# Kernel optimization log

Hardware: AMD Instinct MI355X
Metric: run time of the kernel (lower is better)

Reference implementation:

```python
import jax, jax.numpy as jnp
import numpy as np

B, S, D, H, L = 128, 200, 512, 512, 2  # batch, seq(=max_seq_len), input, hidden, layers


def _uni(key, shape, fan):
    bound = 1.0 / np.sqrt(fan)
    return jax.random.uniform(key, shape, jnp.float32, -bound, bound)


def setup_inputs() -> dict:
    key = jax.random.key(0)
    ks = jax.random.split(key, 12)
    x = jax.random.normal(ks[0], (B, S, D), jnp.float32)
    lens = jax.random.randint(ks[1], (B,), 1, S + 1).astype(jnp.int64)
    return {
        'x': x,
        'lens': lens,
        'Wih_f': _uni(ks[2], (L, 4 * H, D), H),
        'Whh_f': _uni(ks[3], (L, 4 * H, H), H),
        'bih_f': _uni(ks[4], (L, 4 * H), H),
        'bhh_f': _uni(ks[5], (L, 4 * H), H),
        'Wih_b': _uni(ks[6], (L, 4 * H, D), H),
        'Whh_b': _uni(ks[7], (L, 4 * H, H), H),
        'bih_b': _uni(ks[8], (L, 4 * H), H),
        'bhh_b': _uni(ks[9], (L, 4 * H), H),
    }


def _lstm_dir(xs, Wih, Whh, bih, bhh, reverse):
    # xs: [B,S,Din]. Precompute batched input projection, scan the recurrence.
    gx = jnp.einsum('bsd,gd->bsg', xs, Wih) + bih  # [B,S,4H]
    h0 = jnp.zeros((xs.shape[0], Whh.shape[1]), xs.dtype)
    c0 = jnp.zeros_like(h0)

    def step(carry, g_t):
        h, c = carry
        gates = g_t + h @ Whh.T + bhh
        i, f, g, o = jnp.split(gates, 4, axis=-1)  # PyTorch LSTMCell order
        i = jax.nn.sigmoid(i)
        f = jax.nn.sigmoid(f)
        g = jnp.tanh(g)
        o = jax.nn.sigmoid(o)
        c = f * c + i * g
        h = o * jnp.tanh(c)
        return (h, c), h

    _, hs = jax.lax.scan(step, (h0, c0), jnp.swapaxes(gx, 0, 1), reverse=reverse)
    return jnp.swapaxes(hs, 0, 1)  # [B,S,H], time-ordered


def reference(x, lens, Wih_f, Whh_f, bih_f, bhh_f, Wih_b, Whh_b, bih_b, bhh_b):
    valid = (jnp.arange(S)[None, :] < lens[:, None]).astype(x.dtype)[..., None]  # [B,S,1]
    f_in, b_in = x, x
    for l in range(L):
        f_h = _lstm_dir(f_in, Wih_f[l], Whh_f[l], bih_f[l], bhh_f[l], reverse=False)
        b_h = _lstm_dir(b_in, Wih_b[l], Whh_b[l], bih_b[l], bhh_b[l], reverse=True)
        f_h = f_h * valid  # masked_fill(mask, 0) for positions >= lens
        b_h = b_h * valid
        f_in, b_in = f_h, b_h
    return jnp.concatenate((f_in, b_in), axis=2)  # [B,S,2H]
```

## Files before the change

### kernel.cpp

```cpp
#include <hip/hip_runtime.h>
#include <hip/hip_bf16.h>

typedef __bf16 bf16x8 __attribute__((ext_vector_type(8)));
typedef _Float16 f16x8 __attribute__((ext_vector_type(8)));
typedef float f32x4 __attribute__((ext_vector_type(4)));

__device__ __forceinline__ unsigned short f2bf(float f) {
    unsigned int u = __builtin_bit_cast(unsigned int, f);
    u += 0x7FFFu + ((u >> 16) & 1u);
    return (unsigned short)(u >> 16);
}
__device__ __forceinline__ float bf2f(unsigned short s) {
    unsigned int u = ((unsigned int)s) << 16;
    return __builtin_bit_cast(float, u);
}

__device__ __forceinline__ void ldg_c(uint4& d, const void* p) {
    asm volatile("global_load_dwordx4 %0, %1, off sc0 sc1" : "=v"(d) : "v"(p));
}
__device__ __forceinline__ void stg_c32(void* p, unsigned v) {
    asm volatile("global_store_dword %0, %1, off sc0 sc1" :: "v"(p), "v"(v) : "memory");
}
__device__ __forceinline__ void vm_drain() {
    asm volatile("s_waitcnt vmcnt(0)" ::: "memory");
    __builtin_amdgcn_sched_barrier(0);
}
__device__ __forceinline__ void lds_fence() {
    asm volatile("s_waitcnt lgkmcnt(0)" ::: "memory");
    __builtin_amdgcn_sched_barrier(0);
}

__device__ __forceinline__ void wait_flags(const unsigned* f, unsigned tgt) {
    int lane = threadIdx.x & 63;
    for (;;) {
        unsigned v = __hip_atomic_load(f + lane, __ATOMIC_RELAXED, __HIP_MEMORY_SCOPE_AGENT);
        if (__all((int)(v >= tgt))) break;
        __builtin_amdgcn_s_sleep(1);
    }
}

__global__ void prep_x(const float* __restrict__ x,
                       unsigned short* __restrict__ xh,
                       unsigned short* __restrict__ xl) {
    int g = blockIdx.x * 256 + threadIdx.x;
    if (g >= 1638400) return;
    int lane = g & 63;
    int kc   = (g >> 6) & 15;
    int nt   = (g >> 10) & 7;
    int t    = g >> 13;
    int batch = nt * 16 + (lane & 15);
    int k = kc * 32 + (lane >> 4) * 8;
    const float* s = x + ((size_t)batch * 200 + t) * 512 + k;
    float4 v0 = *(const float4*)s;
    float4 v1 = *(const float4*)(s + 4);
    float vv[8] = {v0.x, v0.y, v0.z, v0.w, v1.x, v1.y, v1.z, v1.w};
    unsigned int ph[4], pl[4];
    #pragma unroll
    for (int j = 0; j < 4; ++j) {
        float a = vv[2*j], b = vv[2*j+1];
        unsigned short ha = f2bf(a), hb = f2bf(b);
        unsigned short la = f2bf(a - bf2f(ha)), lb = f2bf(b - bf2f(hb));
        ph[j] = (unsigned)ha | ((unsigned)hb << 16);
        pl[j] = (unsigned)la | ((unsigned)lb << 16);
    }
    ((uint4*)xh)[g] = make_uint4(ph[0], ph[1], ph[2], ph[3]);
    ((uint4*)xl)[g] = make_uint4(pl[0], pl[1], pl[2], pl[3]);
}

__global__ void prep_w(const float* __restrict__ W,
                       unsigned short* __restrict__ wprep,
                       int dir, int isHH) {
    int g = blockIdx.x * 256 + threadIdx.x;
    if (g >= 262144) return;
    int lane = g & 63;
    int kc   = (g >> 6) & 15;
    int mt   = (g >> 10) & 1;
    int cu   = (g >> 11) & 63;
    int l    = g >> 17;
    int r = lane & 15;
    int grow = (2 * mt + (r >> 3)) * 512 + cu * 8 + (r & 7);
    int k = kc * 32 + (lane >> 4) * 8;
    const float* s = W + ((size_t)l * 2048 + grow) * 512 + k;
    float4 v0 = *(const float4*)s;
    float4 v1 = *(const float4*)(s + 4);
    float vv[8] = {v0.x, v0.y, v0.z, v0.w, v1.x, v1.y, v1.z, v1.w};
    bool f16fmt = isHH || (l == 1);
    unsigned int ph[4], pl[4];
    #pragma unroll
    for (int j = 0; j < 4; ++j) {
        float a = vv[2*j], b = vv[2*j+1];
        unsigned short ha, hb, la, lb;
        if (f16fmt) {
            _Float16 fa = (_Float16)a, fb = (_Float16)b;
            _Float16 ra = (_Float16)(a - (float)fa), rb = (_Float16)(b - (float)fb);
            ha = __builtin_bit_cast(unsigned short, fa);
            hb = __builtin_bit_cast(unsigned short, fb);
            la = __builtin_bit_cast(unsigned short, ra);
            lb = __builtin_bit_cast(unsigned short, rb);
        } else {
            ha = f2bf(a); hb = f2bf(b);
            la = f2bf(a - bf2f(ha)); lb = f2bf(b - bf2f(hb));
        }
        ph[j] = (unsigned)ha | ((unsigned)hb << 16);
        pl[j] = (unsigned)la | ((unsigned)lb << 16);
    }
    size_t blk = ((size_t)(dir * 2 + l) * 64 + cu) * 8192;
    size_t fH = blk + (size_t)((isHH * 2 + 0) * 2048 + mt * 1024 + kc * 64 + lane);
    size_t fL = blk + (size_t)((isHH * 2 + 1) * 2048 + mt * 1024 + kc * 64 + lane);
    ((uint4*)wprep)[fH] = make_uint4(ph[0], ph[1], ph[2], ph[3]);
    ((uint4*)wprep)[fL] = make_uint4(pl[0], pl[1], pl[2], pl[3]);
}

__global__ void bsum_k(const float* __restrict__ bih_f, const float* __restrict__ bhh_f,
                       const float* __restrict__ bih_b, const float* __restrict__ bhh_b,
                       float* __restrict__ bsum) {
    int i = blockIdx.x * 256 + threadIdx.x;
    if (i < 8192) {
        int dir = i >> 12, rem = i & 4095;
        const float* bi = dir ? bih_b : bih_f;
        const float* bh = dir ? bhh_b : bhh_f;
        bsum[i] = bi[rem] + bh[rem];
    }
}

__global__ void reset_k(uint4* __restrict__ p) {
    int g = blockIdx.x * 256 + threadIdx.x;
    if (g < 131136) p[g] = make_uint4(0, 0, 0, 0);
}

__global__ void __launch_bounds__(512)
lstm_persist(const unsigned short* __restrict__ xh,
             const unsigned short* __restrict__ xl,
             const unsigned short* __restrict__ wprep,
             const float*          __restrict__ bsum,
             unsigned short*       __restrict__ hbuf,
             const int*            __restrict__ lens,
             float*                __restrict__ dout,
             unsigned*             __restrict__ flagv)
{
    extern __shared__ char smem[];
    float* wexch  = (float*)(smem + 131072);
    float* cst    = (float*)(smem + 131072 + 17408);
    float* bias_l = (float*)(smem + 131072 + 17408 + 4224);

    const int bid  = blockIdx.x;
    const int xcd  = bid & 7;
    const int unit = xcd >> 1;
    const int slot = unit >> 1, dir = unit & 1;
    const int cu8  = ((xcd & 1) << 5) | (bid >> 3);
    const int hj0  = cu8 * 8;
    const int tid  = threadIdx.x;
    const int lane = tid & 63, ng = tid >> 6;
    const int l15  = lane & 15, kg = lane >> 4;
    const int wsel = dir * 2 + slot;

    const int sib = slot ? dir : (2 + dir);
    unsigned* own_f = flagv + unit * 64;
    unsigned* sib_f = flagv + sib * 64;

    {
        const uint4* src = (const uint4*)wprep + ((size_t)(wsel * 64 + cu8) * 8192);
        uint4* dst = (uint4*)smem;
        #pragma unroll
        for (int i = 0; i < 16; ++i) dst[tid + i * 512] = src[tid + i * 512];
    }
    for (int i = tid; i < 8 * 132; i += 512) cst[i] = 0.f;
    if (tid < 32) bias_l[tid] = bsum[wsel * 2048 + (tid >> 3) * 512 + hj0 + (tid & 7)];
    __syncthreads();

    const int lenv = lens[ng * 16 + l15];
    const int gb   = ng * 16 + l15;
    const int u0   = kg * 2;
    const size_t lofs = (size_t)lane * 8;
    const size_t hoff = ((size_t)(ng * 16 + (cu8 >> 2)) * 64 + (cu8 & 3) * 16 + l15) * 8 + u0;
    float* wex = wexch + ng * 32 * 17;

    for (int tau = 0; tau <= 200; ++tau) {
        const int t = slot ? (tau - 1) : tau;
        const bool active = (t >= 0 && t <= 199);
        int t_eff = 0, p_w = 0, p_r = 0;
        if (active) { t_eff = dir ? (199 - t) : t; p_w = t & 3; p_r = (t + 3) & 3; }

        f32x4 acc0 = {0.f, 0.f, 0.f, 0.f};
        f32x4 acc1 = {0.f, 0.f, 0.f, 0.f};

        if (slot == 0 && active) {
            const unsigned short* XH = xh + (size_t)t_eff * 65536;
            const unsigned short* XL = xl + (size_t)t_eff * 65536;
            #pragma unroll
            for (int kc = 0; kc < 16; ++kc) {
                size_t bo = (size_t)ng * 8192 + (size_t)kc * 512 + lofs;
                bf16x8 bxh = *(const bf16x8*)(XH + bo);
                bf16x8 bxl = *(const bf16x8*)(XL + bo);
                const char* ab = smem + kc * 1024 + lane * 16;
                bf16x8 aih0 = *(const bf16x8*)(ab);
                bf16x8 ail0 = *(const bf16x8*)(ab + 32768);
                bf16x8 aih1 = *(const bf16x8*)(ab + 16384);
                bf16x8 ail1 = *(const bf16x8*)(ab + 16384 + 32768);
                acc0 = __builtin_amdgcn_mfma_f32_16x16x32_bf16(aih0, bxh, acc0, 0, 0, 0);
                acc0 = __builtin_amdgcn_mfma_f32_16x16x32_bf16(aih0, bxl, acc0, 0, 0, 0);
                acc0 = __builtin_amdgcn_mfma_f32_16x16x32_bf16(ail0, bxh, acc0, 0, 0, 0);
                acc1 = __builtin_amdgcn_mfma_f32_16x16x32_bf16(aih1, bxh, acc1, 0, 0, 0);
                acc1 = __builtin_amdgcn_mfma_f32_16x16x32_bf16(aih1, bxl, acc1, 0, 0, 0);
                acc1 = __builtin_amdgcn_mfma_f32_16x16x32_bf16(ail1, bxh, acc1, 0, 0, 0);
            }
        }

        {
            unsigned tgt = (unsigned)tau;
            if (ng == 0) wait_flags(own_f, tgt);
            if (slot == 1) { if (ng == 1) wait_flags(sib_f, tgt); }
            else if (tau >= 3) { if (ng == 1) wait_flags(sib_f, tgt - 2); }
        }
        __syncthreads();

        if (active) {
            const unsigned short* HH = hbuf + ((size_t)((slot * 4 + p_r) * 2 + dir) << 16);

            if (slot == 0) {
                uint4 vh[16];
                #pragma unroll
                for (int kc = 0; kc < 16; ++kc)
                    ldg_c(vh[kc], HH + (size_t)ng * 8192 + (size_t)kc * 512 + lofs);
                vm_drain();
                #pragma unroll
                for (int kc = 0; kc < 16; ++kc) {
                    f16x8 bh = __builtin_bit_cast(f16x8, vh[kc]);
                    const char* ab = smem + kc * 1024 + lane * 16;
                    f16x8 ahh0 = *(const f16x8*)(ab + 65536);
                    f16x8 ahl0 = *(const f16x8*)(ab + 98304);
                    f16x8 ahh1 = *(const f16x8*)(ab + 16384 + 65536);
                    f16x8 ahl1 = *(const f16x8*)(ab + 16384 + 98304);
                    acc0 = __builtin_amdgcn_mfma_f32_16x16x32_f16(ahh0, bh, acc0, 0, 0, 0);
                    acc0 = __builtin_amdgcn_mfma_f32_16x16x32_f16(ahl0, bh, acc0, 0, 0, 0);
                    acc1 = __builtin_amdgcn_mfma_f32_16x16x32_f16(ahh1, bh, acc1, 0, 0, 0);
                    acc1 = __builtin_amdgcn_mfma_f32_16x16x32_f16(ahl1, bh, acc1, 0, 0, 0);
                }
            } else {
                int p_x = t & 3;
                const unsigned short* XHc = hbuf + ((size_t)(p_x * 2 + dir) << 16);
                uint4 vx[16], vh[16];
                #pragma unroll
                for (int kc = 0; kc < 16; ++kc) {
                    size_t bo = (size_t)ng * 8192 + (size_t)kc * 512 + lofs;
                    ldg_c(vx[kc], XHc + bo);
                    ldg_c(vh[kc], HH + bo);
                }
                vm_drain();
                const bool mv = (t_eff < lenv);
                #pragma unroll
                for (int kc = 0; kc < 16; ++kc) {
                    if (!mv) vx[kc] = make_uint4(0, 0, 0, 0);
                    f16x8 xv = __builtin_bit_cast(f16x8, vx[kc]);
                    f16x8 bh = __builtin_bit_cast(f16x8, vh[kc]);
                    const char* ab = smem + kc * 1024 + lane * 16;
                    f16x8 aih0 = *(const f16x8*)(ab);
                    f16x8 ahh0 = *(const f16x8*)(ab + 65536);
                    f16x8 ahl0 = *(const f16x8*)(ab + 98304);
                    f16x8 aih1 = *(const f16x8*)(ab + 16384);
                    f16x8 ahh1 = *(const f16x8*)(ab + 16384 + 65536);
                    f16x8 ahl1 = *(const f16x8*)(ab + 16384 + 98304);
                    acc0 = __builtin_amdgcn_mfma_f32_16x16x32_f16(aih0, xv, acc0, 0, 0, 0);
                    acc0 = __builtin_amdgcn_mfma_f32_16x16x32_f16(ahh0, bh, acc0, 0, 0, 0);
                    acc0 = __builtin_amdgcn_mfma_f32_16x16x32_f16(ahl0, bh, acc0, 0, 0, 0);
                    acc1 = __builtin_amdgcn_mfma_f32_16x16x32_f16(aih1, xv, acc1, 0, 0, 0);
                    acc1 = __builtin_amdgcn_mfma_f32_16x16x32_f16(ahh1, bh, acc1, 0, 0, 0);
                    acc1 = __builtin_amdgcn_mfma_f32_16x16x32_f16(ahl1, bh, acc1, 0, 0, 0);
                }
            }

            #pragma unroll
            for (int r = 0; r < 4; ++r) {
                wex[(kg * 4 + r) * 17 + l15]      = acc0[r];
                wex[(16 + kg * 4 + r) * 17 + l15] = acc1[r];
            }
            lds_fence();

            unsigned short* Hw = hbuf + ((size_t)((slot * 4 + p_w) * 2 + dir) << 16);
            unsigned hpk = 0;
            float hm0 = 0.f, hm1 = 0.f;
            #pragma unroll
            for (int j = 0; j < 2; ++j) {
                int u = u0 + j;
                float g0 = wex[(0  + u) * 17 + l15] + bias_l[u];
                float g1 = wex[(8  + u) * 17 + l15] + bias_l[8 + u];
                float g2 = wex[(16 + u) * 17 + l15] + bias_l[16 + u];
                float g3 = wex[(24 + u) * 17 + l15] + bias_l[24 + u];
                float cv = cst[u * 132 + gb];
                float iG = 1.f / (1.f + expf(-g0));
                float fG = 1.f / (1.f + expf(-g1));
                float gG = tanhf(g2);
                float oG = 1.f / (1.f + expf(-g3));
                float cn = fG * cv + iG * gG;
                cst[u * 132 + gb] = cn;
                float hn = oG * tanhf(cn);
                _Float16 hf = (_Float16)hn;
                hpk |= ((unsigned)__builtin_bit_cast(unsigned short, hf)) << (16 * j);
                float hm = (t_eff < lenv) ? hn : 0.f;
                if (j) hm1 = hm; else hm0 = hm;
            }
            stg_c32(Hw + hoff, hpk);
            if (slot) {
                float2 o = make_float2(hm0, hm1);
                *(float2*)(dout + ((size_t)gb * 200 + t_eff) * 1024 + dir * 512 + hj0 + u0) = o;
            }
            vm_drain();
        }

        __syncthreads();
        if (tid == 0)
            __hip_atomic_store(own_f + cu8, (unsigned)(tau + 1),
                               __ATOMIC_RELAXED, __HIP_MEMORY_SCOPE_AGENT);
    }
}

extern "C" void kernel_launch(void* const* d_in, const int* in_sizes, int n_in,
                              void* d_out, int out_size, void* d_ws, size_t ws_size,
                              hipStream_t stream) {
    const float* x     = (const float*)d_in[0];
    const int*   lens  = (const int*)d_in[1];
    const float* Wih_f = (const float*)d_in[2];
    const float* Whh_f = (const float*)d_in[3];
    const float* bih_f = (const float*)d_in[4];
    const float* bhh_f = (const float*)d_in[5];
    const float* Wih_b = (const float*)d_in[6];
    const float* Whh_b = (const float*)d_in[7];
    const float* bih_b = (const float*)d_in[8];
    const float* bhh_b = (const float*)d_in[9];
    float* out = (float*)d_out;
    char* ws = (char*)d_ws;
    if (ws_size < 88114176) return;

    unsigned short* xh    = (unsigned short*)(ws);
    unsigned short* xl    = (unsigned short*)(ws + 26214400);
    unsigned short* wprep = (unsigned short*)(ws + 52428800);
    float*          bsum  = (float*)(ws + 85983232);
    unsigned short* hbuf  = (unsigned short*)(ws + 86016000);
    unsigned*       flg   = (unsigned*)(ws + 88113152);

    prep_x<<<6400, 256, 0, stream>>>(x, xh, xl);
    prep_w<<<1024, 256, 0, stream>>>(Wih_f, wprep, 0, 0);
    prep_w<<<1024, 256, 0, stream>>>(Whh_f, wprep, 0, 1);
    prep_w<<<1024, 256, 0, stream>>>(Wih_b, wprep, 1, 0);
    prep_w<<<1024, 256, 0, stream>>>(Whh_b, wprep, 1, 1);
    bsum_k<<<32, 256, 0, stream>>>(bih_f, bhh_f, bih_b, bhh_b, bsum);
    reset_k<<<513, 256, 0, stream>>>((uint4*)hbuf);

    static const int LDS_BYTES = 131072 + 17408 + 4224 + 128;
    hipFuncSetAttribute(reinterpret_cast<const void*>(lstm_persist),
                        hipFuncAttributeMaxDynamicSharedMemorySize, LDS_BYTES);

    void* args[] = {(void*)&xh, (void*)&xl, (void*)&wprep, (void*)&bsum,
                    (void*)&hbuf, (void*)&lens, (void*)&out, (void*)&flg};
    hipLaunchCooperativeKernel(reinterpret_cast<void*>(lstm_persist),
                               dim3(256), dim3(512), args, LDS_BYTES, stream);
}
```

Before: 1.774 ms.

## Add deep-history mode storing every hidden step to remove ring-buffer backpressure waits

Adds a templated DEEP variant that writes each timestep's hidden state to its own slot in a full-length history stream instead of a 4-deep ring buffer. Layer 0 no longer waits on layer 1's progress, and since written slots are never overwritten, reads use plain cached loads instead of coherent sc0/sc1 loads with explicit drains. The t=0 recurrent matmul is skipped. It needs much more workspace, overwrites the weight-prep area (so weights are loaded to LDS first and a startup flag barrier is added), and only runs when ws_size is large enough.

```diff
diff --git a/kernel.cpp b/kernel.cpp
--- a/kernel.cpp
+++ b/kernel.cpp
@@ -123,11 +123,12 @@
     }
 }
 
-__global__ void reset_k(uint4* __restrict__ p) {
+__global__ void reset_k(uint4* __restrict__ p, int n) {
     int g = blockIdx.x * 256 + threadIdx.x;
-    if (g < 131136) p[g] = make_uint4(0, 0, 0, 0);
-}
-
+    if (g < n) p[g] = make_uint4(0, 0, 0, 0);
+}
+
+template<int DEEP>
 __global__ void __launch_bounds__(512)
 lstm_persist(const unsigned short* __restrict__ xh,
              const unsigned short* __restrict__ xl,
@@ -136,7 +137,8 @@
              unsigned short*       __restrict__ hbuf,
              const int*            __restrict__ lens,
              float*                __restrict__ dout,
-             unsigned*             __restrict__ flagv)
+             unsigned*             __restrict__ flagv,
+             unsigned*             __restrict__ sflg)
 {
     extern __shared__ char smem[];
     float* wexch  = (float*)(smem + 131072);
@@ -158,7 +160,20 @@
     unsigned* own_f = flagv + unit * 64;
     unsigned* sib_f = flagv + sib * 64;
 
-    {
+    unsigned short* own_stream = hbuf + (size_t)unit * 13107200;
+    const unsigned short* x_stream = hbuf + (size_t)dir * 13107200;
+
+    if constexpr (DEEP) {
+        const unsigned short* src = wprep + (size_t)(wsel * 64 + cu8) * 65536;
+        uint4 v[16];
+        #pragma unroll
+        for (int i = 0; i < 16; ++i)
+            ldg_c(v[i], src + (size_t)(tid + i * 512) * 8);
+        vm_drain();
+        uint4* dst = (uint4*)smem;
+        #pragma unroll
+        for (int i = 0; i < 16; ++i) dst[tid + i * 512] = v[i];
+    } else {
         const uint4* src = (const uint4*)wprep + ((size_t)(wsel * 64 + cu8) * 8192);
         uint4* dst = (uint4*)smem;
         #pragma unroll
@@ -167,6 +182,14 @@
     for (int i = tid; i < 8 * 132; i += 512) cst[i] = 0.f;
     if (tid < 32) bias_l[tid] = bsum[wsel * 2048 + (tid >> 3) * 512 + hj0 + (tid & 7)];
     __syncthreads();
+
+    if constexpr (DEEP) {
+        if (tid == 0)
+            __hip_atomic_store(sflg + unit * 64 + cu8, 1u,
+                               __ATOMIC_RELAXED, __HIP_MEMORY_SCOPE_AGENT);
+        if (slot == 0 && ng < 4) wait_flags(sflg + ng * 64, 1u);
+        __syncthreads();
+    }
 
     const int lenv = lens[ng * 16 + l15];
     const int gb   = ng * 16 + l15;
@@ -210,62 +233,96 @@
             unsigned tgt = (unsigned)tau;
             if (ng == 0) wait_flags(own_f, tgt);
             if (slot == 1) { if (ng == 1) wait_flags(sib_f, tgt); }
-            else if (tau >= 3) { if (ng == 1) wait_flags(sib_f, tgt - 2); }
+            else if constexpr (!DEEP) {
+                if (ng == 1 && tau >= 3) wait_flags(sib_f, tgt - 2);
+            }
         }
         __syncthreads();
 
         if (active) {
-            const unsigned short* HH = hbuf + ((size_t)((slot * 4 + p_r) * 2 + dir) << 16);
+            const unsigned short* HH;
+            if constexpr (DEEP)
+                HH = own_stream + (size_t)(t > 0 ? t - 1 : 0) * 65536;
+            else
+                HH = hbuf + ((size_t)((slot * 4 + p_r) * 2 + dir) << 16);
+            const bool do_hh = DEEP ? (t > 0) : true;
 
             if (slot == 0) {
-                uint4 vh[16];
-                #pragma unroll
-                for (int kc = 0; kc < 16; ++kc)
-                    ldg_c(vh[kc], HH + (size_t)ng * 8192 + (size_t)kc * 512 + lofs);
-                vm_drain();
-                #pragma unroll
-                for (int kc = 0; kc < 16; ++kc) {
-                    f16x8 bh = __builtin_bit_cast(f16x8, vh[kc]);
-                    const char* ab = smem + kc * 1024 + lane * 16;
-                    f16x8 ahh0 = *(const f16x8*)(ab + 65536);
-                    f16x8 ahl0 = *(const f16x8*)(ab + 98304);
-                    f16x8 ahh1 = *(const f16x8*)(ab + 16384 + 65536);
-                    f16x8 ahl1 = *(const f16x8*)(ab + 16384 + 98304);
-                    acc0 = __builtin_amdgcn_mfma_f32_16x16x32_f16(ahh0, bh, acc0, 0, 0, 0);
-                    acc0 = __builtin_amdgcn_mfma_f32_16x16x32_f16(ahl0, bh, acc0, 0, 0, 0);
-                    acc1 = __builtin_amdgcn_mfma_f32_16x16x32_f16(ahh1, bh, acc1, 0, 0, 0);
-                    acc1 = __builtin_amdgcn_mfma_f32_16x16x32_f16(ahl1, bh, acc1, 0, 0, 0);
+                if (do_hh) {
+                    uint4 vh[16];
+                    if constexpr (DEEP) {
+                        #pragma unroll
+                        for (int kc = 0; kc < 16; ++kc)
+                            vh[kc] = *(const uint4*)(HH + (size_t)ng * 8192 + (size_t)kc * 512 + lofs);
+                    } else {
+                        #pragma unroll
+                        for (int kc = 0; kc < 16; ++kc)
+                            ldg_c(vh[kc], HH + (size_t)ng * 8192 + (size_t)kc * 512 + lofs);
+                        vm_drain();
+                    }
+                    #pragma unroll
+                    for (int kc = 0; kc < 16; ++kc) {
+                        f16x8 bh = __builtin_bit_cast(f16x8, vh[kc]);
+                        const char* ab = smem + kc * 1024 + lane * 16;
+                        f16x8 ahh0 = *(const f16x8*)(ab + 65536);
+                        f16x8 ahl0 = *(const f16x8*)(ab + 98304);
+                        f16x8 ahh1 = *(const f16x8*)(ab + 16384 + 65536);
+                        f16x8 ahl1 = *(const f16x8*)(ab + 16384 + 98304);
+                        acc0 = __builtin_amdgcn_mfma_f32_16x16x32_f16(ahh0, bh, acc0, 0, 0, 0);
+                        acc0 = __builtin_amdgcn_mfma_f32_16x16x32_f16(ahl0, bh, acc0, 0, 0, 0);
+                        acc1 = __builtin_amdgcn_mfma_f32_16x16x32_f16(ahh1, bh, acc1, 0, 0, 0);
+                        acc1 = __builtin_amdgcn_mfma_f32_16x16x32_f16(ahl1, bh, acc1, 0, 0, 0);
+                    }
                 }
             } else {
-                int p_x = t & 3;
-                const unsigned short* XHc = hbuf + ((size_t)(p_x * 2 + dir) << 16);
+                const unsigned short* XHc;
+                if constexpr (DEEP)
+                    XHc = x_stream + (size_t)t * 65536;
+                else
+                    XHc = hbuf + ((size_t)((t & 3) * 2 + dir) << 16);
+
                 uint4 vx[16], vh[16];
-                #pragma unroll
-                for (int kc = 0; kc < 16; ++kc) {
-                    size_t bo = (size_t)ng * 8192 + (size_t)kc * 512 + lofs;
-                    ldg_c(vx[kc], XHc + bo);
-                    ldg_c(vh[kc], HH + bo);
+                if constexpr (DEEP) {
+                    #pragma unroll
+                    for (int kc = 0; kc < 16; ++kc) {
+                        size_t bo = (size_t)ng * 8192 + (size_t)kc * 512 + lofs;
+                        vx[kc] = *(const uint4*)(XHc + bo);
+                        if (do_hh) vh[kc] = *(const uint4*)(HH + bo);
+                    }
+                } else {
+                    #pragma unroll
+                    for (int kc = 0; kc < 16; ++kc) {
+                        size_t bo = (size_t)ng * 8192 + (size_t)kc * 512 + lofs;
+                        ldg_c(vx[kc], XHc + bo);
+                        ldg_c(vh[kc], HH + bo);
+                    }
+                    vm_drain();
                 }
-                vm_drain();
                 const bool mv = (t_eff < lenv);
                 #pragma unroll
                 for (int kc = 0; kc < 16; ++kc) {
                     if (!mv) vx[kc] = make_uint4(0, 0, 0, 0);
                     f16x8 xv = __builtin_bit_cast(f16x8, vx[kc]);
-                    f16x8 bh = __builtin_bit_cast(f16x8, vh[kc]);
                     const char* ab = smem + kc * 1024 + lane * 16;
                     f16x8 aih0 = *(const f16x8*)(ab);
-                    f16x8 ahh0 = *(const f16x8*)(ab + 65536);
-                    f16x8 ahl0 = *(const f16x8*)(ab + 98304);
                     f16x8 aih1 = *(const f16x8*)(ab + 16384);
-                    f16x8 ahh1 = *(const f16x8*)(ab + 16384 + 65536);
-                    f16x8 ahl1 = *(const f16x8*)(ab + 16384 + 98304);
                     acc0 = __builtin_amdgcn_mfma_f32_16x16x32_f16(aih0, xv, acc0, 0, 0, 0);
-                    acc0 = __builtin_amdgcn_mfma_f32_16x16x32_f16(ahh0, bh, acc0, 0, 0, 0);
-                    acc0 = __builtin_amdgcn_mfma_f32_16x16x32_f16(ahl0, bh, acc0, 0, 0, 0);
                     acc1 = __builtin_amdgcn_mfma_f32_16x16x32_f16(aih1, xv, acc1, 0, 0, 0);
-                    acc1 = __builtin_amdgcn_mfma_f32_16x16x32_f16(ahh1, bh, acc1, 0, 0, 0);
-                    acc1 = __builtin_amdgcn_mfma_f32_16x16x32_f16(ahl1, bh, acc1, 0, 0, 0);
+                }
+                if (do_hh) {
+                    #pragma unroll
+                    for (int kc = 0; kc < 16; ++kc) {
+                        f16x8 bh = __builtin_bit_cast(f16x8, vh[kc]);
+                        const char* ab = smem + kc * 1024 + lane * 16;
+                        f16x8 ahh0 = *(const f16x8*)(ab + 65536);
+                        f16x8 ahl0 = *(const f16x8*)(ab + 98304);
+                        f16x8 ahh1 = *(const f16x8*)(ab + 16384 + 65536);
+                        f16x8 ahl1 = *(const f16x8*)(ab + 16384 + 98304);
+                        acc0 = __builtin_amdgcn_mfma_f32_16x16x32_f16(ahh0, bh, acc0, 0, 0, 0);
+                        acc0 = __builtin_amdgcn_mfma_f32_16x16x32_f16(ahl0, bh, acc0, 0, 0, 0);
+                        acc1 = __builtin_amdgcn_mfma_f32_16x16x32_f16(ahh1, bh, acc1, 0, 0, 0);
+                        acc1 = __builtin_amdgcn_mfma_f32_16x16x32_f16(ahl1, bh, acc1, 0, 0, 0);
+                    }
                 }
             }
 
@@ -276,7 +333,11 @@
             }
             lds_fence();
 
-            unsigned short* Hw = hbuf + ((size_t)((slot * 4 + p_w) * 2 + dir) << 16);
+            unsigned short* Hw;
+            if constexpr (DEEP)
+                Hw = own_stream + (size_t)t * 65536;
+            else
+                Hw = hbuf + ((size_t)((slot * 4 + p_w) * 2 + dir) << 16);
             unsigned hpk = 0;
             float hm0 = 0.f, hm1 = 0.f;
             #pragma unroll
@@ -329,14 +390,25 @@
     const float* bhh_b = (const float*)d_in[9];
     float* out = (float*)d_out;
     char* ws = (char*)d_ws;
-    if (ws_size < 88114176) return;
+
+    const bool deep = (ws_size >= 157321216);
+    if (!deep && ws_size < 88114176) return;
 
     unsigned short* xh    = (unsigned short*)(ws);
     unsigned short* xl    = (unsigned short*)(ws + 26214400);
     unsigned short* wprep = (unsigned short*)(ws + 52428800);
-    float*          bsum  = (float*)(ws + 85983232);
-    unsigned short* hbuf  = (unsigned short*)(ws + 86016000);
-    unsigned*       flg   = (unsigned*)(ws + 88113152);
+    float* bsum; unsigned short* hbuf; unsigned *flg, *sflg;
+    if (deep) {
+        hbuf = (unsigned short*)(ws + 52428800);
+        bsum = (float*)(ws + 157286400);
+        flg  = (unsigned*)(ws + 157319168);
+        sflg = (unsigned*)(ws + 157320192);
+    } else {
+        bsum = (float*)(ws + 85983232);
+        hbuf = (unsigned short*)(ws + 86016000);
+        flg  = (unsigned*)(ws + 88113152);
+        sflg = flg;
+    }
 
     prep_x<<<6400, 256, 0, stream>>>(x, xh, xl);
     prep_w<<<1024, 256, 0, stream>>>(Wih_f, wprep, 0, 0);
@@ -344,14 +416,18 @@
     prep_w<<<1024, 256, 0, stream>>>(Wih_b, wprep, 1, 0);
     prep_w<<<1024, 256, 0, stream>>>(Whh_b, wprep, 1, 1);
     bsum_k<<<32, 256, 0, stream>>>(bih_f, bhh_f, bih_b, bhh_b, bsum);
-    reset_k<<<513, 256, 0, stream>>>((uint4*)hbuf);
+    if (deep)
+        reset_k<<<1, 256, 0, stream>>>((uint4*)flg, 128);
+    else
+        reset_k<<<513, 256, 0, stream>>>((uint4*)hbuf, 131136);
 
     static const int LDS_BYTES = 131072 + 17408 + 4224 + 128;
-    hipFuncSetAttribute(reinterpret_cast<const void*>(lstm_persist),
+    void* k = deep ? reinterpret_cast<void*>(lstm_persist<1>)
+                   : reinterpret_cast<void*>(lstm_persist<0>);
+    hipFuncSetAttribute(reinterpret_cast<const void*>(k),
                         hipFuncAttributeMaxDynamicSharedMemorySize, LDS_BYTES);
 
     void* args[] = {(void*)&xh, (void*)&xl, (void*)&wprep, (void*)&bsum,
-                    (void*)&hbuf, (void*)&lens, (void*)&out, (void*)&flg};
-    hipLaunchCooperativeKernel(reinterpret_cast<void*>(lstm_persist),
-                               dim3(256), dim3(512), args, LDS_BYTES, stream);
-}
+                    (void*)&hbuf, (void*)&lens, (void*)&out, (void*)&flg, (void*)&sflg};
+    hipLaunchCooperativeKernel(k, dim3(256), dim3(512), args, LDS_BYTES, stream);
+}
```

Result: slower. 1.837 ms (+3.6%).
